# Kernel optimization log

Measured on AMD Instinct MI355X. Metric: run time of the kernel, lower is better.

## Reference

```python
import jax, jax.numpy as jnp
import numpy as np

DIM = 1024
HEADS = 16
EPS = 1e-5


def layer_norm(x, gamma, beta):
    mu = jnp.mean(x, axis=-1, keepdims=True)
    var = jnp.mean(jnp.square(x - mu), axis=-1, keepdims=True)
    return (x - mu) * jax.lax.rsqrt(var + EPS) * gamma + beta


def setup_inputs() -> dict:
    key = jax.random.key(0)
    ks = jax.random.split(key, 9)
    B, Nq, Nk = 8, 1024, 1024
    s = 1.0 / np.sqrt(DIM)
    return {
        "x": jax.random.normal(ks[0], (B, Nq, DIM), jnp.float32),
        "context": jax.random.normal(ks[1], (B, Nk, DIM), jnp.float32),
        "relative_position_bias": jax.random.normal(ks[2], (HEADS, Nq, Nk), jnp.float32),
        "Wq": jax.random.normal(ks[3], (DIM, DIM), jnp.float32) * s,
        "Wk": jax.random.normal(ks[4], (DIM, DIM), jnp.float32) * s,
        "Wv": jax.random.normal(ks[5], (DIM, DIM), jnp.float32) * s,
        "Wo": jax.random.normal(ks[6], (DIM, DIM), jnp.float32) * s,
        "bo": jnp.zeros((DIM,), jnp.float32),
        "gamma": jnp.ones((DIM,), jnp.float32),
        "beta": jnp.zeros((DIM,), jnp.float32),
    }


def reference(x, context, relative_position_bias, Wq, Wk, Wv, Wo, bo, gamma, beta):
    h = HEADS
    d = DIM // h
    scale = d ** -0.5
    xn = layer_norm(x, gamma, beta)
    cn = layer_norm(context, gamma, beta)
    B, Nq, _ = x.shape
    Nk = context.shape[1]
    # b n (h d) -> b h n d
    q = (xn @ Wq).reshape(B, Nq, h, d).transpose(0, 2, 1, 3)
    k = (cn @ Wk).reshape(B, Nk, h, d).transpose(0, 2, 1, 3)
    v = (cn @ Wv).reshape(B, Nk, h, d).transpose(0, 2, 1, 3)
    scores = jnp.einsum('bhid,bhjd->bhij', q, k) * scale
    scores = scores + relative_position_bias[None]
    attn = jax.nn.softmax(scores, axis=-1)
    out = jnp.einsum('bhij,bhjd->bhid', attn, v)
    out = out.transpose(0, 2, 1, 3).reshape(B, Nq, h * d)
    return out @ Wo + bo
```

## Files before the change

### kernel.cpp

```cpp
#include <hip/hip_runtime.h>
#include <hip/hip_bf16.h>
#include <stdint.h>

#define DIM   1024
#define HEADS 16
#define HD    64
#define NB    8
#define NTOK  1024
#define MROWS (NB*NTOK)

#define LOG2E 1.4426950408889634f
#define SCL   (0.125f * LOG2E)

typedef __attribute__((ext_vector_type(8))) _Float16 f16x8;
typedef __attribute__((ext_vector_type(4))) _Float16 f16x4;
typedef __attribute__((ext_vector_type(4))) float    f32x4;

typedef unsigned int uint_as1 __attribute__((address_space(1)));
typedef unsigned int uint_as3 __attribute__((address_space(3)));

__device__ __forceinline__ void gload16(const void* g, void* l) {
    __builtin_amdgcn_global_load_lds((const uint_as1*)g, (uint_as3*)l, 16, 0, 0);
}

__device__ __forceinline__ unsigned pkrtz(float a, float b) {
    auto h = __builtin_amdgcn_cvt_pkrtz(a, b);
    return __builtin_bit_cast(unsigned, h);
}

#if __has_builtin(__builtin_amdgcn_permlane32_swap)
__device__ __forceinline__ void swap32(unsigned& a, unsigned& b) {
    auto r = __builtin_amdgcn_permlane32_swap(a, b, false, false);
    a = r[0]; b = r[1];
}
#else
__device__ __forceinline__ void swap32(unsigned& a, unsigned& b) {
    unsigned as = (unsigned)__shfl_xor((int)a, 32, 64);
    unsigned bs = (unsigned)__shfl_xor((int)b, 32, 64);
    bool lo = ((threadIdx.x & 63) < 32);
    unsigned na = lo ? a : bs, nb = lo ? as : b;
    a = na; b = nb;
}
#endif
#if __has_builtin(__builtin_amdgcn_permlane16_swap)
__device__ __forceinline__ void swap16(unsigned& a, unsigned& b) {
    auto r = __builtin_amdgcn_permlane16_swap(a, b, false, false);
    a = r[0]; b = r[1];
}
#else
__device__ __forceinline__ void swap16(unsigned& a, unsigned& b) {
    unsigned as = (unsigned)__shfl_xor((int)a, 16, 64);
    unsigned bs = (unsigned)__shfl_xor((int)b, 16, 64);
    bool ev = ((threadIdx.x & 16) == 0);
    unsigned na = ev ? a : bs, nb = ev ? as : b;
    a = na; b = nb;
}
#endif
__device__ __forceinline__ float redsum32(float x) {
    unsigned a = __builtin_bit_cast(unsigned, x), b = a;
    swap32(a, b);
    return __builtin_bit_cast(float, a) + __builtin_bit_cast(float, b);
}
__device__ __forceinline__ float redsum16(float x) {
    unsigned a = __builtin_bit_cast(unsigned, x), b = a;
    swap16(a, b);
    return __builtin_bit_cast(float, a) + __builtin_bit_cast(float, b);
}

__global__ __launch_bounds__(256) void prep_kernel(const float* __restrict__ x,
                                                   const float* __restrict__ ctx,
                                                   const float* __restrict__ gamma,
                                                   const float* __restrict__ beta,
                                                   _Float16* __restrict__ xn,
                                                   _Float16* __restrict__ cn,
                                                   const float* __restrict__ Wq, const float* __restrict__ Wk,
                                                   const float* __restrict__ Wv, const float* __restrict__ Wo,
                                                   _Float16* __restrict__ Tq, _Float16* __restrict__ Tk,
                                                   _Float16* __restrict__ Tv, _Float16* __restrict__ To,
                                                   const float* __restrict__ bias,
                                                   _Float16* __restrict__ bias2) {
    __shared__ float redm[8];
    __shared__ float tile[32][33];
    int bid = blockIdx.x;
    int t = threadIdx.x;
    if (bid < 2 * MROWS) {
        int row = bid;
        const float* src; _Float16* dst;
        if (row < MROWS) { src = x + (size_t)row * DIM;   dst = xn + (size_t)row * DIM; }
        else             { int r = row - MROWS;
                           src = ctx + (size_t)r * DIM;   dst = cn + (size_t)r * DIM; }
        float4 v = *(const float4*)(src + t * 4);
        float s  = v.x + v.y + v.z + v.w;
        float s2 = v.x*v.x + v.y*v.y + v.z*v.z + v.w*v.w;
        #pragma unroll
        for (int o = 32; o; o >>= 1) { s += __shfl_xor(s, o, 64); s2 += __shfl_xor(s2, o, 64); }
        int w = t >> 6, l = t & 63;
        if (l == 0) { redm[w] = s; redm[4 + w] = s2; }
        __syncthreads();
        s  = redm[0] + redm[1] + redm[2] + redm[3];
        s2 = redm[4] + redm[5] + redm[6] + redm[7];
        float mu   = s * (1.0f / DIM);
        float rstd = rsqrtf(s2 * (1.0f / DIM) - mu * mu + 1e-5f);
        float4 g  = *(const float4*)(gamma + t * 4);
        float4 bb = *(const float4*)(beta  + t * 4);
        f16x4 o;
        o[0] = (_Float16)((v.x - mu) * rstd * g.x + bb.x);
        o[1] = (_Float16)((v.y - mu) * rstd * g.y + bb.y);
        o[2] = (_Float16)((v.z - mu) * rstd * g.z + bb.z);
        o[3] = (_Float16)((v.w - mu) * rstd * g.w + bb.w);
        *(f16x4*)(dst + t * 4) = o;
    } else if (bid < 2 * MROWS + 4096) {
        int fid = bid - 2 * MROWS;
        int m = fid >> 10;
        int rem = fid & 1023;
        int j0 = (rem & 31) * 32, k0 = (rem >> 5) * 32;
        const float* W = (m == 0) ? Wq : (m == 1) ? Wk : (m == 2) ? Wv : Wo;
        _Float16*    T = (m == 0) ? Tq : (m == 1) ? Tk : (m == 2) ? Tv : To;
        int tx = t & 31, ty = t >> 5;
        #pragma unroll
        for (int i = 0; i < 4; i++) tile[ty + i*8][tx] = W[(size_t)(k0 + ty + i*8) * DIM + j0 + tx];
        __syncthreads();
        #pragma unroll
        for (int i = 0; i < 4; i++) T[(size_t)(j0 + ty + i*8) * DIM + k0 + tx] = (_Float16)tile[tx][ty + i*8];
    } else {
        size_t i = ((size_t)(bid - 2 * MROWS - 4096) * 256 + t) * 8;
        float4 a = *(const float4*)(bias + i);
        float4 b = *(const float4*)(bias + i + 4);
        f16x8 o;
        o[0] = (_Float16)(a.x * LOG2E); o[1] = (_Float16)(a.y * LOG2E);
        o[2] = (_Float16)(a.z * LOG2E); o[3] = (_Float16)(a.w * LOG2E);
        o[4] = (_Float16)(b.x * LOG2E); o[5] = (_Float16)(b.y * LOG2E);
        o[6] = (_Float16)(b.z * LOG2E); o[7] = (_Float16)(b.w * LOG2E);
        *(f16x8*)(bias2 + i) = o;
    }
}

__global__ __launch_bounds__(256) void biasconv_kernel(const float* __restrict__ bias,
                                                       _Float16* __restrict__ bias2) {
    size_t i = ((size_t)blockIdx.x * 256 + threadIdx.x) * 8;
    float4 a = *(const float4*)(bias + i);
    float4 b = *(const float4*)(bias + i + 4);
    f16x8 o;
    o[0] = (_Float16)(a.x * LOG2E); o[1] = (_Float16)(a.y * LOG2E);
    o[2] = (_Float16)(a.z * LOG2E); o[3] = (_Float16)(a.w * LOG2E);
    o[4] = (_Float16)(b.x * LOG2E); o[5] = (_Float16)(b.y * LOG2E);
    o[6] = (_Float16)(b.z * LOG2E); o[7] = (_Float16)(b.w * LOG2E);
    *(f16x8*)(bias2 + i) = o;
}

__global__ __launch_bounds__(256) void gemm_qkv(const _Float16* __restrict__ xn,
                                                const _Float16* __restrict__ cn,
                                                const _Float16* __restrict__ wqT,
                                                const _Float16* __restrict__ wkT,
                                                const _Float16* __restrict__ wvT,
                                                _Float16* __restrict__ qbf,
                                                _Float16* __restrict__ kbf,
                                                _Float16* __restrict__ vtb) {
    __shared__ _Float16 As[128 * 64];
    __shared__ _Float16 Bs[128 * 64];
    const int K = DIM;
    int mode = blockIdx.y >> 3;
    int n0 = (blockIdx.y & 7) * 128;
    int m0 = blockIdx.x * 128;
    const _Float16* A  = (mode == 0) ? xn : cn;
    const _Float16* BT = (mode == 0) ? wqT : (mode == 1) ? wkT : wvT;
    int t = threadIdx.x, w = t >> 6, l = t & 63;
    int wr = w >> 1, wc = w & 1, ln = l & 15, qtr = l >> 4;
    f32x4 acc[4][4] = {};
    int srow = w * 8 + (l >> 3);
    int cg   = (l & 7) ^ (srow & 7);
    const _Float16* Ag = A  + (size_t)(m0 + srow) * K + cg * 8;
    const _Float16* Bg = BT + (size_t)(n0 + srow) * K + cg * 8;
    for (int kt = 0; kt < K; kt += 64) {
        #pragma unroll
        for (int p = 0; p < 4; p++) {
            gload16(Ag + (size_t)(p * 32) * K, &As[(p * 32 + w * 8) * 64]);
            gload16(Bg + (size_t)(p * 32) * K, &Bs[(p * 32 + w * 8) * 64]);
        }
        Ag += 64; Bg += 64;
        __syncthreads();
        #pragma unroll
        for (int kk = 0; kk < 2; kk++) {
            f16x8 af[4], bfr[4];
            #pragma unroll
            for (int r = 0; r < 4; r++)
                af[r]  = *(const f16x8*)&As[(wr * 64 + r * 16 + ln) * 64 + (((qtr + kk*4) ^ (ln & 7)) * 8)];
            #pragma unroll
            for (int c = 0; c < 4; c++)
                bfr[c] = *(const f16x8*)&Bs[(wc * 64 + c * 16 + ln) * 64 + (((qtr + kk*4) ^ (ln & 7)) * 8)];
            #pragma unroll
            for (int r = 0; r < 4; r++)
                #pragma unroll
                for (int c = 0; c < 4; c++)
                    acc[r][c] = __builtin_amdgcn_mfma_f32_16x16x32_f16(af[r], bfr[c], acc[r][c], 0, 0, 0);
        }
        __syncthreads();
    }
    #pragma unroll
    for (int r = 0; r < 4; r++)
        #pragma unroll
        for (int c = 0; c < 4; c++) {
            int gn = n0 + wc * 64 + c * 16 + ln;
            int h = gn >> 6, d = gn & 63;
            #pragma unroll
            for (int q = 0; q < 4; q++) {
                int gm = m0 + wr * 64 + r * 16 + qtr * 4 + q;
                int b = gm >> 10, n = gm & 1023;
                float v = acc[r][c][q];
                if (mode == 0)
                    qbf[(((size_t)(b * HEADS + h) * NTOK + n) << 6) + d] = (_Float16)(v * SCL);
                else if (mode == 1)
                    kbf[(((size_t)(b * HEADS + h) * NTOK + n) << 6) + d] = (_Float16)v;
                else
                    vtb[(((size_t)(b * HEADS + h) * HD + d) << 10) + n] = (_Float16)v;
            }
        }
}

__global__ __launch_bounds__(256) void gemm_out(const _Float16* __restrict__ A,
                                                const _Float16* __restrict__ BT,
                                                float* __restrict__ Cout,
                                                const float* __restrict__ bias) {
    __shared__ _Float16 As[128 * 64];
    __shared__ _Float16 Bs[128 * 64];
    const int K = DIM;
    int m0 = blockIdx.x * 128, n0 = blockIdx.y * 128;
    int t = threadIdx.x, w = t >> 6, l = t & 63;
    int wr = w >> 1, wc = w & 1, ln = l & 15, qtr = l >> 4;
    f32x4 acc[4][4] = {};
    int srow = w * 8 + (l >> 3);
    int cg   = (l & 7) ^ (srow & 7);
    const _Float16* Ag = A  + (size_t)(m0 + srow) * K + cg * 8;
    const _Float16* Bg = BT + (size_t)(n0 + srow) * K + cg * 8;
    for (int kt = 0; kt < K; kt += 64) {
        #pragma unroll
        for (int p = 0; p < 4; p++) {
            gload16(Ag + (size_t)(p * 32) * K, &As[(p * 32 + w * 8) * 64]);
            gload16(Bg + (size_t)(p * 32) * K, &Bs[(p * 32 + w * 8) * 64]);
        }
        Ag += 64; Bg += 64;
        __syncthreads();
        #pragma unroll
        for (int kk = 0; kk < 2; kk++) {
            f16x8 af[4], bfr[4];
            #pragma unroll
            for (int r = 0; r < 4; r++)
                af[r]  = *(const f16x8*)&As[(wr * 64 + r * 16 + ln) * 64 + (((qtr + kk*4) ^ (ln & 7)) * 8)];
            #pragma unroll
            for (int c = 0; c < 4; c++)
                bfr[c] = *(const f16x8*)&Bs[(wc * 64 + c * 16 + ln) * 64 + (((qtr + kk*4) ^ (ln & 7)) * 8)];
            #pragma unroll
            for (int r = 0; r < 4; r++)
                #pragma unroll
                for (int c = 0; c < 4; c++)
                    acc[r][c] = __builtin_amdgcn_mfma_f32_16x16x32_f16(af[r], bfr[c], acc[r][c], 0, 0, 0);
        }
        __syncthreads();
    }
    #pragma unroll
    for (int r = 0; r < 4; r++)
        #pragma unroll
        for (int c = 0; c < 4; c++) {
            int gn = n0 + wc * 64 + c * 16 + ln;
            float bv = bias[gn];
            #pragma unroll
            for (int q = 0; q < 4; q++) {
                int gm = m0 + wr * 64 + r * 16 + qtr * 4 + q;
                Cout[(size_t)gm * DIM + gn] = acc[r][c][q] + bv;
            }
        }
}

__global__ __launch_bounds__(256) void attn_kernel(const _Float16* __restrict__ qb,
                                                   const _Float16* __restrict__ kb,
                                                   const _Float16* __restrict__ vt,
                                                   const _Float16* __restrict__ bias2,
                                                   _Float16* __restrict__ ao) {
    __shared__ _Float16 Kt[2][64 * 64];
    __shared__ _Float16 Vs[2][64 * 64];
    int bid = blockIdx.x;
    int rem = bid >> 3;
    int h = (bid & 7) * 2 + (rem & 1);
    int b = (rem >> 1) & 7;
    int qt = rem >> 4;
    int q0 = qt * 64;
    int t = threadIdx.x, w = t >> 6, l = t & 63, ln = l & 15, qtr = l >> 4;
    const _Float16* qbase = qb + (size_t)(b * HEADS + h) * NTOK * HD;
    const _Float16* kbase = kb + (size_t)(b * HEADS + h) * NTOK * HD;
    const _Float16* vbase = vt + (size_t)(b * HEADS + h) * HD * NTOK;
    const _Float16* bbase = bias2 + ((size_t)h * NTOK + q0 + w * 16) * NTOK;

    f16x8 qfr[2];
    #pragma unroll
    for (int ks = 0; ks < 2; ks++)
        qfr[ks] = *(const f16x8*)&qbase[(size_t)(q0 + w*16 + ln) * HD + ks*32 + qtr*8];

#define STAGE(BUF, J0) do {                                                     \
        int rb_ = w * 16;                                                       \
        _Float16* kl_ = &Kt[BUF][rb_ * 64];                                     \
        _Float16* vl_ = &Vs[BUF][rb_ * 64];                                     \
        int r_ = rb_ + (l >> 3); int cg_ = (l & 7) ^ (r_ & 7);                  \
        gload16(kbase + (size_t)((J0) + r_) * HD + cg_ * 8, kl_);               \
        gload16(vbase + (size_t)r_ * NTOK + (J0) + cg_ * 8, vl_);               \
        r_ += 8; cg_ = (l & 7) ^ (r_ & 7);                                      \
        gload16(kbase + (size_t)((J0) + r_) * HD + cg_ * 8, kl_ + 8 * 64);      \
        gload16(vbase + (size_t)r_ * NTOK + (J0) + cg_ * 8, vl_ + 8 * 64);      \
    } while (0)

#define LOADB(DST, TT) do {                                                     \
        _Pragma("unroll")                                                       \
        for (int r_ = 0; r_ < 4; r_++)                                          \
            DST[r_] = *(const f16x4*)&bbase[(size_t)ln * NTOK                   \
                                            + (TT)*64 + qtr*4 + r_*16];         \
    } while (0)

    STAGE(0, 0);
    f16x4 bpp[2][4];
    LOADB(bpp[0], 0);
    __syncthreads();

    float l_part = 0.f;
    f32x4 acc[4] = {};

    #pragma unroll 2
    for (int tt = 0; tt < 16; tt++) {
        int cur = tt & 1;
        if (tt < 15) { STAGE(cur ^ 1, (tt + 1) * 64); LOADB(bpp[cur ^ 1], tt + 1); }

        f32x4 st2[4];
        #pragma unroll
        for (int r = 0; r < 4; r++) {
            f16x4 bb = bpp[cur][r];
            f32x4 ci = {(float)bb[0], (float)bb[1], (float)bb[2], (float)bb[3]};
            st2[r] = ci;
        }
        __builtin_amdgcn_s_setprio(1);
        #pragma unroll
        for (int r = 0; r < 4; r++) {
            int row = r * 16 + ln;
            #pragma unroll
            for (int ks = 0; ks < 2; ks++) {
                f16x8 kf = *(const f16x8*)&Kt[cur][row * 64 + (((qtr + ks*4) ^ (ln & 7)) * 8)];
                st2[r] = __builtin_amdgcn_mfma_f32_16x16x32_f16(kf, qfr[ks], st2[r], 0, 0, 0);
            }
        }
        __builtin_amdgcn_s_setprio(0);

        float sig = 0.f;
        unsigned pk2[4][2];
        #pragma unroll
        for (int r = 0; r < 4; r++) {
            float p0 = exp2f(st2[r][0]);
            float p1 = exp2f(st2[r][1]);
            float p2 = exp2f(st2[r][2]);
            float p3 = exp2f(st2[r][3]);
            sig += (p0 + p1) + (p2 + p3);
            pk2[r][0] = pkrtz(p0, p1);
            pk2[r][1] = pkrtz(p2, p3);
        }
        l_part += sig;

        f16x8 pfr[2];
        #pragma unroll
        for (int ks = 0; ks < 2; ks++) {
            unsigned pw[4];
            #pragma unroll
            for (int c = 0; c < 2; c++) {
                unsigned U = pk2[2*ks][c], T = pk2[2*ks + 1][c];
                swap32(U, T);
                swap16(U, T);
                pw[c]     = U;
                pw[2 + c] = T;
            }
            pfr[ks] = __builtin_bit_cast(f16x8, *(const uint4*)pw);
        }

        __builtin_amdgcn_s_setprio(1);
        #pragma unroll
        for (int dg = 0; dg < 4; dg++) {
            int row = dg * 16 + ln;
            #pragma unroll
            for (int ks = 0; ks < 2; ks++) {
                f16x8 vf = *(const f16x8*)&Vs[cur][row * 64 + (((qtr + ks*4) ^ (ln & 7)) * 8)];
                acc[dg] = __builtin_amdgcn_mfma_f32_16x16x32_f16(pfr[ks], vf, acc[dg], 0, 0, 0);
            }
        }
        __builtin_amdgcn_s_setprio(0);
        __syncthreads();
    }

    float inv = 1.0f / redsum16(redsum32(l_part));
    float invm[4];
    #pragma unroll
    for (int m = 0; m < 4; m++) invm[m] = __shfl(inv, (l & 48) | (qtr * 4 + m), 64);
    size_t rowb = (size_t)b * NTOK + q0 + w * 16 + qtr * 4;
    #pragma unroll
    for (int dg = 0; dg < 4; dg++)
        #pragma unroll
        for (int m = 0; m < 4; m++)
            ao[(rowb + m) * DIM + h * HD + dg * 16 + ln] = (_Float16)(acc[dg][m] * invm[m]);
#undef STAGE
#undef LOADB
}

extern "C" void kernel_launch(void* const* d_in, const int* in_sizes, int n_in,
                              void* d_out, int out_size, void* d_ws, size_t ws_size,
                              hipStream_t stream) {
    const float* x     = (const float*)d_in[0];
    const float* ctx   = (const float*)d_in[1];
    const float* bias  = (const float*)d_in[2];
    const float* Wq    = (const float*)d_in[3];
    const float* Wk    = (const float*)d_in[4];
    const float* Wv    = (const float*)d_in[5];
    const float* Wo    = (const float*)d_in[6];
    const float* bo    = (const float*)d_in[7];
    const float* gamma = (const float*)d_in[8];
    const float* beta  = (const float*)d_in[9];
    float* out = (float*)d_out;

    _Float16* ws  = (_Float16*)d_ws;
    _Float16* xn  = ws;
    _Float16* cn  = xn  + (size_t)MROWS * DIM;
    _Float16* wqT = cn  + (size_t)MROWS * DIM;
    _Float16* wkT = wqT + (size_t)DIM * DIM;
    _Float16* wvT = wkT + (size_t)DIM * DIM;
    _Float16* woT = wvT + (size_t)DIM * DIM;
    _Float16* qbf = woT + (size_t)DIM * DIM;
    _Float16* kbf = qbf + (size_t)MROWS * DIM;
    _Float16* vtb = kbf + (size_t)MROWS * DIM;
    _Float16* aob = vtb + (size_t)MROWS * DIM;
    _Float16* wsEnd = aob + (size_t)MROWS * DIM;

    const size_t biasElems = (size_t)HEADS * NTOK * NTOK;
    const size_t needBytes = ((size_t)(wsEnd - ws) + biasElems) * sizeof(_Float16);
    bool roomy = ws_size >= needBytes;
    _Float16* bias2 = roomy ? wsEnd : ws;

    int prepBlocks = 2 * MROWS + 4096 + (roomy ? 8192 : 0);
    prep_kernel<<<dim3(prepBlocks), dim3(256), 0, stream>>>(
        x, ctx, gamma, beta, xn, cn, Wq, Wk, Wv, Wo, wqT, wkT, wvT, woT, bias, bias2);
    gemm_qkv<<<dim3(64, 24), dim3(256), 0, stream>>>(xn, cn, wqT, wkT, wvT, qbf, kbf, vtb);
    if (!roomy)
        biasconv_kernel<<<dim3(8192), dim3(256), 0, stream>>>(bias, bias2);
    attn_kernel<<<dim3(NB * HEADS * 16), dim3(256), 0, stream>>>(qbf, kbf, vtb, bias2, aob);
    gemm_out<<<dim3(64, 8), dim3(256), 0, stream>>>(aob, woT, out, bo);
}
```

Measured before the change: 228.7 us.

## Software-pipeline QK^T one tile ahead with triple-buffered V in attention

Restructures the attention loop so the QK^T MFMAs for tile t+1 are issued while tile t's softmax exponentials and PV MFMAs run. V gets a third LDS buffer and K/V loads are staged two tiles ahead, with the barrier moved to the top of the loop. The row-sum accumulation now uses packed fp16 dot2 instructions on the already-converted probabilities rather than separate fp32 adds. The loop is fully unrolled, which raises register pressure and code size and may lower occupancy.

```diff
diff --git a/kernel.cpp b/kernel.cpp
--- a/kernel.cpp
+++ b/kernel.cpp
@@ -27,6 +27,19 @@
     auto h = __builtin_amdgcn_cvt_pkrtz(a, b);
     return __builtin_bit_cast(unsigned, h);
 }
+
+#if __has_builtin(__builtin_amdgcn_fdot2)
+__device__ __forceinline__ float dot2acc(unsigned p, float c) {
+    auto one2 = __builtin_amdgcn_cvt_pkrtz(1.0f, 1.0f);
+    return __builtin_amdgcn_fdot2(__builtin_bit_cast(decltype(one2), p), one2, c, false);
+}
+#else
+__device__ __forceinline__ float dot2acc(unsigned p, float c) {
+    _Float16 lo = __builtin_bit_cast(_Float16, (unsigned short)(p & 0xffff));
+    _Float16 hi = __builtin_bit_cast(_Float16, (unsigned short)(p >> 16));
+    return c + (float)lo + (float)hi;
+}
+#endif
 
 #if __has_builtin(__builtin_amdgcn_permlane32_swap)
 __device__ __forceinline__ void swap32(unsigned& a, unsigned& b) {
@@ -277,7 +290,7 @@
                                                    const _Float16* __restrict__ bias2,
                                                    _Float16* __restrict__ ao) {
     __shared__ _Float16 Kt[2][64 * 64];
-    __shared__ _Float16 Vs[2][64 * 64];
+    __shared__ _Float16 Vs[3][64 * 64];
     int bid = blockIdx.x;
     int rem = bid >> 3;
     int h = (bid & 7) * 2 + (rem & 1);
@@ -295,10 +308,10 @@
     for (int ks = 0; ks < 2; ks++)
         qfr[ks] = *(const f16x8*)&qbase[(size_t)(q0 + w*16 + ln) * HD + ks*32 + qtr*8];
 
-#define STAGE(BUF, J0) do {                                                     \
+#define STAGEKV(KB, VB, J0) do {                                                \
         int rb_ = w * 16;                                                       \
-        _Float16* kl_ = &Kt[BUF][rb_ * 64];                                     \
-        _Float16* vl_ = &Vs[BUF][rb_ * 64];                                     \
+        _Float16* kl_ = &Kt[KB][rb_ * 64];                                      \
+        _Float16* vl_ = &Vs[VB][rb_ * 64];                                      \
         int r_ = rb_ + (l >> 3); int cg_ = (l & 7) ^ (r_ & 7);                  \
         gload16(kbase + (size_t)((J0) + r_) * HD + cg_ * 8, kl_);               \
         gload16(vbase + (size_t)r_ * NTOK + (J0) + cg_ * 8, vl_);               \
@@ -314,39 +327,44 @@
                                             + (TT)*64 + qtr*4 + r_*16];         \
     } while (0)
 
-    STAGE(0, 0);
+#define QKT(ST, BUFK, BPP) do {                                                 \
+        _Pragma("unroll")                                                       \
+        for (int r_ = 0; r_ < 4; r_++) {                                        \
+            f16x4 bb_ = BPP[r_];                                                \
+            f32x4 ci_ = {(float)bb_[0], (float)bb_[1], (float)bb_[2], (float)bb_[3]}; \
+            ST[r_] = ci_;                                                       \
+        }                                                                       \
+        __builtin_amdgcn_s_setprio(1);                                          \
+        _Pragma("unroll")                                                       \
+        for (int r_ = 0; r_ < 4; r_++) {                                        \
+            int row_ = r_ * 16 + ln;                                            \
+            _Pragma("unroll")                                                   \
+            for (int ks_ = 0; ks_ < 2; ks_++) {                                 \
+                f16x8 kf_ = *(const f16x8*)&Kt[BUFK][row_ * 64 + (((qtr + ks_*4) ^ (ln & 7)) * 8)]; \
+                ST[r_] = __builtin_amdgcn_mfma_f32_16x16x32_f16(kf_, qfr[ks_], ST[r_], 0, 0, 0); \
+            }                                                                   \
+        }                                                                       \
+        __builtin_amdgcn_s_setprio(0);                                          \
+    } while (0)
+
+    STAGEKV(0, 0, 0);
     f16x4 bpp[2][4];
     LOADB(bpp[0], 0);
     __syncthreads();
+    STAGEKV(1, 1, 64);
+    LOADB(bpp[1], 1);
+    f32x4 st2[4], st2b[4];
+    QKT(st2, 0, bpp[0]);
 
     float l_part = 0.f;
     f32x4 acc[4] = {};
 
-    #pragma unroll 2
+    #pragma unroll
     for (int tt = 0; tt < 16; tt++) {
-        int cur = tt & 1;
-        if (tt < 15) { STAGE(cur ^ 1, (tt + 1) * 64); LOADB(bpp[cur ^ 1], tt + 1); }
-
-        f32x4 st2[4];
-        #pragma unroll
-        for (int r = 0; r < 4; r++) {
-            f16x4 bb = bpp[cur][r];
-            f32x4 ci = {(float)bb[0], (float)bb[1], (float)bb[2], (float)bb[3]};
-            st2[r] = ci;
-        }
-        __builtin_amdgcn_s_setprio(1);
-        #pragma unroll
-        for (int r = 0; r < 4; r++) {
-            int row = r * 16 + ln;
-            #pragma unroll
-            for (int ks = 0; ks < 2; ks++) {
-                f16x8 kf = *(const f16x8*)&Kt[cur][row * 64 + (((qtr + ks*4) ^ (ln & 7)) * 8)];
-                st2[r] = __builtin_amdgcn_mfma_f32_16x16x32_f16(kf, qfr[ks], st2[r], 0, 0, 0);
-            }
-        }
-        __builtin_amdgcn_s_setprio(0);
-
-        float sig = 0.f;
+        __syncthreads();
+        if (tt < 14) STAGEKV(tt & 1, (tt + 2) % 3, (tt + 2) * 64);
+
+        float sig = l_part;
         unsigned pk2[4][2];
         #pragma unroll
         for (int r = 0; r < 4; r++) {
@@ -354,11 +372,12 @@
             float p1 = exp2f(st2[r][1]);
             float p2 = exp2f(st2[r][2]);
             float p3 = exp2f(st2[r][3]);
-            sig += (p0 + p1) + (p2 + p3);
             pk2[r][0] = pkrtz(p0, p1);
             pk2[r][1] = pkrtz(p2, p3);
-        }
-        l_part += sig;
+            sig = dot2acc(pk2[r][0], sig);
+            sig = dot2acc(pk2[r][1], sig);
+        }
+        l_part = sig;
 
         f16x8 pfr[2];
         #pragma unroll
@@ -375,18 +394,24 @@
             pfr[ks] = __builtin_bit_cast(f16x8, *(const uint4*)pw);
         }
 
+        if (tt < 15) QKT(st2b, (tt + 1) & 1, bpp[(tt + 1) & 1]);
+        if (tt < 14) LOADB(bpp[tt & 1], tt + 2);
+
         __builtin_amdgcn_s_setprio(1);
         #pragma unroll
         for (int dg = 0; dg < 4; dg++) {
             int row = dg * 16 + ln;
             #pragma unroll
             for (int ks = 0; ks < 2; ks++) {
-                f16x8 vf = *(const f16x8*)&Vs[cur][row * 64 + (((qtr + ks*4) ^ (ln & 7)) * 8)];
+                f16x8 vf = *(const f16x8*)&Vs[tt % 3][row * 64 + (((qtr + ks*4) ^ (ln & 7)) * 8)];
                 acc[dg] = __builtin_amdgcn_mfma_f32_16x16x32_f16(pfr[ks], vf, acc[dg], 0, 0, 0);
             }
         }
         __builtin_amdgcn_s_setprio(0);
-        __syncthreads();
+
+        if (tt < 15) {
+            st2[0] = st2b[0]; st2[1] = st2b[1]; st2[2] = st2b[2]; st2[3] = st2b[3];
+        }
     }
 
     float inv = 1.0f / redsum16(redsum32(l_part));
@@ -399,8 +424,9 @@
         #pragma unroll
         for (int m = 0; m < 4; m++)
             ao[(rowb + m) * DIM + h * HD + dg * 16 + ln] = (_Float16)(acc[dg][m] * invm[m]);
-#undef STAGE
+#undef STAGEKV
 #undef LOADB
+#undef QKT
 }
 
 extern "C" void kernel_launch(void* const* d_in, const int* in_sizes, int n_in,
```

Result: no change. 229.9 us (+0.5%).

## Triple-buffer K/V tiles with prefetch depth two and fdot2 row-sum accumulation

Applied to the files above, without the earlier changes.

The attention kernel moves from double to triple LDS buffering of K/V tiles, issuing loads two tiles ahead. __syncthreads is replaced by explicit s_waitcnt vmcnt plus s_barrier so outstanding global loads can stay in flight across iterations. The softmax denominator is now accumulated from the packed fp16 probabilities with fdot2 against ones instead of fp32 adds. The extra LDS per block may reduce occupancy, and the hand-counted vmcnt values must match the number of loads issued. Summing the rounded fp16 values also changes numerics slightly.

```diff
diff --git a/kernel.cpp b/kernel.cpp
--- a/kernel.cpp
+++ b/kernel.cpp
@@ -27,6 +27,19 @@
     auto h = __builtin_amdgcn_cvt_pkrtz(a, b);
     return __builtin_bit_cast(unsigned, h);
 }
+
+#if __has_builtin(__builtin_amdgcn_fdot2)
+__device__ __forceinline__ float dot2acc(unsigned p, float c) {
+    auto one2 = __builtin_amdgcn_cvt_pkrtz(1.0f, 1.0f);
+    return __builtin_amdgcn_fdot2(__builtin_bit_cast(decltype(one2), p), one2, c, false);
+}
+#else
+__device__ __forceinline__ float dot2acc(unsigned p, float c) {
+    _Float16 lo = __builtin_bit_cast(_Float16, (unsigned short)(p & 0xffff));
+    _Float16 hi = __builtin_bit_cast(_Float16, (unsigned short)(p >> 16));
+    return c + (float)lo + (float)hi;
+}
+#endif
 
 #if __has_builtin(__builtin_amdgcn_permlane32_swap)
 __device__ __forceinline__ void swap32(unsigned& a, unsigned& b) {
@@ -276,8 +289,8 @@
                                                    const _Float16* __restrict__ vt,
                                                    const _Float16* __restrict__ bias2,
                                                    _Float16* __restrict__ ao) {
-    __shared__ _Float16 Kt[2][64 * 64];
-    __shared__ _Float16 Vs[2][64 * 64];
+    __shared__ _Float16 Kt[3][64 * 64];
+    __shared__ _Float16 Vs[3][64 * 64];
     int bid = blockIdx.x;
     int rem = bid >> 3;
     int h = (bid & 7) * 2 + (rem & 1);
@@ -295,7 +308,7 @@
     for (int ks = 0; ks < 2; ks++)
         qfr[ks] = *(const f16x8*)&qbase[(size_t)(q0 + w*16 + ln) * HD + ks*32 + qtr*8];
 
-#define STAGE(BUF, J0) do {                                                     \
+#define STAGEKV(BUF, J0) do {                                                   \
         int rb_ = w * 16;                                                       \
         _Float16* kl_ = &Kt[BUF][rb_ * 64];                                     \
         _Float16* vl_ = &Vs[BUF][rb_ * 64];                                     \
@@ -314,26 +327,34 @@
                                             + (TT)*64 + qtr*4 + r_*16];         \
     } while (0)
 
-    STAGE(0, 0);
+    STAGEKV(0, 0);
     f16x4 bpp[2][4];
     LOADB(bpp[0], 0);
-    __syncthreads();
+    STAGEKV(1, 64);
+    LOADB(bpp[1], 1);
+    asm volatile("s_waitcnt vmcnt(8)" ::: "memory");
+    asm volatile("s_barrier" ::: "memory");
 
     float l_part = 0.f;
     f32x4 acc[4] = {};
 
-    #pragma unroll 2
+    #pragma unroll
     for (int tt = 0; tt < 16; tt++) {
-        int cur = tt & 1;
-        if (tt < 15) { STAGE(cur ^ 1, (tt + 1) * 64); LOADB(bpp[cur ^ 1], tt + 1); }
+        int cur = tt % 3;
 
         f32x4 st2[4];
         #pragma unroll
         for (int r = 0; r < 4; r++) {
-            f16x4 bb = bpp[cur][r];
+            f16x4 bb = bpp[tt & 1][r];
             f32x4 ci = {(float)bb[0], (float)bb[1], (float)bb[2], (float)bb[3]};
             st2[r] = ci;
         }
+
+        if (tt < 14) {
+            STAGEKV((tt + 2) % 3, (tt + 2) * 64);
+            LOADB(bpp[tt & 1], tt + 2);
+        }
+
         __builtin_amdgcn_s_setprio(1);
         #pragma unroll
         for (int r = 0; r < 4; r++) {
@@ -346,7 +367,7 @@
         }
         __builtin_amdgcn_s_setprio(0);
 
-        float sig = 0.f;
+        float sig = l_part;
         unsigned pk2[4][2];
         #pragma unroll
         for (int r = 0; r < 4; r++) {
@@ -354,11 +375,12 @@
             float p1 = exp2f(st2[r][1]);
             float p2 = exp2f(st2[r][2]);
             float p3 = exp2f(st2[r][3]);
-            sig += (p0 + p1) + (p2 + p3);
             pk2[r][0] = pkrtz(p0, p1);
             pk2[r][1] = pkrtz(p2, p3);
-        }
-        l_part += sig;
+            sig = dot2acc(pk2[r][0], sig);
+            sig = dot2acc(pk2[r][1], sig);
+        }
+        l_part = sig;
 
         f16x8 pfr[2];
         #pragma unroll
@@ -386,7 +408,14 @@
             }
         }
         __builtin_amdgcn_s_setprio(0);
-        __syncthreads();
+
+        if (tt < 14) {
+            asm volatile("s_waitcnt vmcnt(8)" ::: "memory");
+            asm volatile("s_barrier" ::: "memory");
+        } else if (tt == 14) {
+            asm volatile("s_waitcnt vmcnt(0)" ::: "memory");
+            asm volatile("s_barrier" ::: "memory");
+        }
     }
 
     float inv = 1.0f / redsum16(redsum32(l_part));
@@ -399,7 +428,7 @@
         #pragma unroll
         for (int m = 0; m < 4; m++)
             ao[(rowb + m) * DIM + h * HD + dg * 16 + ln] = (_Float16)(acc[dg][m] * invm[m]);
-#undef STAGE
+#undef STAGEKV
 #undef LOADB
 }
 
```

Result: slower. 241.3 us (+5.5%).
